# Kernel optimization log

Hardware: AMD Instinct MI355X
Metric: run time of the kernel (lower is better)

The kernel has to match this reference:

```python
import jax, jax.numpy as jnp
import numpy as np


def setup_inputs() -> dict:
    key = jax.random.key(0)
    k1, k2 = jax.random.split(key)
    x = jax.random.normal(k1, (4, 2048, 512), dtype=jnp.float32)
    proxy = jax.random.normal(k2, (16, 512), dtype=jnp.float32)
    return {"x": x, "proxy": proxy}


def reference(x, proxy):
    # x: (B, S, D), proxy: (P, D)
    num_proxies = proxy.shape[0]
    # prods: (B, P, S) = proxy @ x^T per batch
    prods = jnp.einsum('pd,bsd->bps', proxy, x)
    # broadcast outer product: (B, P, S, D), then running prefix sum over seq
    y = jnp.cumsum(prods[..., None] * x[:, None, :, :], axis=2)
    # softmax gate over proxies (dim=1), scaled by sqrt(P)
    w = jax.nn.softmax(prods / jnp.sqrt(jnp.float32(num_proxies)), axis=1)
    # weighted sum over proxies -> (B, S, D)
    out = jnp.einsum('bps,bpsd->bsd', w, y)
    return out
```

## Files before the change

### kernel.cpp

```cpp
#include <hip/hip_runtime.h>
#include <hip/hip_bf16.h>

#define B 4
#define S 2048
#define D 512
#define P 16
#define NC 64
#define CL 32

__global__ __launch_bounds__(256) void k_prods(const float* __restrict__ x,
                                               const float* __restrict__ proxy,
                                               float* __restrict__ prods,
                                               float* __restrict__ wgt) {
    const int wave = (blockIdx.x * blockDim.x + threadIdx.x) >> 6;
    const int lane = threadIdx.x & 63;
    const int bs0  = wave * 4;

    float4 pA[P], pB[P];
#pragma unroll
    for (int p = 0; p < P; ++p) {
        const float* pr = proxy + p * D + lane * 8;
        pA[p] = *(const float4*)pr;
        pB[p] = *(const float4*)(pr + 4);
    }

#pragma unroll
    for (int r = 0; r < 4; ++r) {
        const int bs = bs0 + r;
        const float* xr = x + (size_t)bs * D + lane * 8;
        float4 xa = *(const float4*)xr;
        float4 xb = *(const float4*)(xr + 4);

        float part[P];
#pragma unroll
        for (int p = 0; p < P; ++p) {
            part[p] = xa.x*pA[p].x + xa.y*pA[p].y + xa.z*pA[p].z + xa.w*pA[p].w
                    + xb.x*pB[p].x + xb.y*pB[p].y + xb.z*pB[p].z + xb.w*pB[p].w;
        }

        float a8[8];
#pragma unroll
        for (int k = 0; k < 8; ++k) {
            bool hi = lane & 1;
            float mine = hi ? part[2*k+1] : part[2*k];
            float oth  = hi ? part[2*k]   : part[2*k+1];
            a8[k] = mine + __shfl_xor(oth, 1);
        }
        float a4[4];
#pragma unroll
        for (int k = 0; k < 4; ++k) {
            bool hi = lane & 2;
            float mine = hi ? a8[2*k+1] : a8[2*k];
            float oth  = hi ? a8[2*k]   : a8[2*k+1];
            a4[k] = mine + __shfl_xor(oth, 2);
        }
        float a2[2];
#pragma unroll
        for (int k = 0; k < 2; ++k) {
            bool hi = lane & 4;
            float mine = hi ? a4[2*k+1] : a4[2*k];
            float oth  = hi ? a4[2*k]   : a4[2*k+1];
            a2[k] = mine + __shfl_xor(oth, 4);
        }
        float a1;
        {
            bool hi = lane & 8;
            float mine = hi ? a2[1] : a2[0];
            float oth  = hi ? a2[0] : a2[1];
            a1 = mine + __shfl_xor(oth, 8);
        }
        a1 += __shfl_xor(a1, 16);
        a1 += __shfl_xor(a1, 32);

        float m = a1;
#pragma unroll
        for (int off = 1; off < 16; off <<= 1) m = fmaxf(m, __shfl_xor(m, off));
        float e = __expf((a1 - m) * 0.25f);
        float den = e;
#pragma unroll
        for (int off = 1; off < 16; off <<= 1) den += __shfl_xor(den, off);

        if (lane < P) {
            prods[(size_t)bs * P + lane] = a1;
            wgt  [(size_t)bs * P + lane] = e / den;
        }
    }
}

__global__ __launch_bounds__(256) void k_totals(const float* __restrict__ x,
                                                const float* __restrict__ prods,
                                                float* __restrict__ T) {
    int h = blockIdx.x & 1;
    int c = (blockIdx.x >> 1) & (NC - 1);
    int b = blockIdx.x >> 7;
    int d = h * 256 + threadIdx.x;

    float acc[P];
#pragma unroll
    for (int p = 0; p < P; ++p) acc[p] = 0.f;

    int bs0 = b * S + c * CL;
#pragma unroll 4
    for (int i = 0; i < CL; ++i) {
        int bs = bs0 + i;
        float xv = x[(size_t)bs * D + d];
        const float4* pp = (const float4*)(prods + (size_t)bs * P);
        float pr[P];
        ((float4*)pr)[0] = pp[0];
        ((float4*)pr)[1] = pp[1];
        ((float4*)pr)[2] = pp[2];
        ((float4*)pr)[3] = pp[3];
#pragma unroll
        for (int p = 0; p < P; ++p) acc[p] = fmaf(pr[p], xv, acc[p]);
    }
    size_t tb = ((size_t)(b * NC + c)) * (P * D) + d;
#pragma unroll
    for (int p = 0; p < P; ++p) T[tb + p * D] = acc[p];
}

__global__ __launch_bounds__(256) void k_scan(float* __restrict__ T) {
    int t = blockIdx.x * blockDim.x + threadIdx.x;
    int d = t & (D - 1);
    int p = (t >> 9) & (P - 1);
    int b = t >> 13;
    size_t base = ((size_t)b * NC * P + p) * D + d;
    float run = 0.f;
#pragma unroll 8
    for (int c = 0; c < NC; ++c) {
        size_t idx = base + (size_t)c * (P * D);
        float v = T[idx];
        T[idx] = run;
        run += v;
    }
}

__global__ __launch_bounds__(256) void k_apply(const float* __restrict__ x,
                                               const float* __restrict__ prods,
                                               const float* __restrict__ wgt,
                                               const float* __restrict__ T,
                                               float* __restrict__ out) {
    __shared__ float s_pw[2][CL][P];

    int h = blockIdx.x & 1;
    int c = (blockIdx.x >> 1) & (NC - 1);
    int b = blockIdx.x >> 7;
    int d = h * 256 + threadIdx.x;
    int bs0 = b * S + c * CL;

    {
        int t = threadIdx.x;
        if (t < 128) {
            ((float4*)&s_pw[0][0][0])[t] =
                ((const float4*)(prods + (size_t)bs0 * P))[t];
        } else {
            ((float4*)&s_pw[1][0][0])[t - 128] =
                ((const float4*)(wgt + (size_t)bs0 * P))[t - 128];
        }
    }

    float xv[CL];
#pragma unroll
    for (int i = 0; i < CL; ++i) xv[i] = x[(size_t)(bs0 + i) * D + d];

    float st[P];
    size_t tb = ((size_t)(b * NC + c)) * (P * D) + d;
#pragma unroll
    for (int p = 0; p < P; ++p) st[p] = T[tb + p * D];

    __syncthreads();

#pragma unroll
    for (int i = 0; i < CL; ++i) {
        float pr[P], ww[P];
        const float4* sp = (const float4*)&s_pw[0][i][0];
        const float4* sw = (const float4*)&s_pw[1][i][0];
        ((float4*)pr)[0] = sp[0];
        ((float4*)pr)[1] = sp[1];
        ((float4*)pr)[2] = sp[2];
        ((float4*)pr)[3] = sp[3];
        ((float4*)ww)[0] = sw[0];
        ((float4*)ww)[1] = sw[1];
        ((float4*)ww)[2] = sw[2];
        ((float4*)ww)[3] = sw[3];
        float o = 0.f;
#pragma unroll
        for (int p = 0; p < P; ++p) {
            st[p] = fmaf(pr[p], xv[i], st[p]);
            o = fmaf(ww[p], st[p], o);
        }
        out[(size_t)(bs0 + i) * D + d] = o;
    }
}

extern "C" void kernel_launch(void* const* d_in, const int* in_sizes, int n_in,
                              void* d_out, int out_size, void* d_ws, size_t ws_size,
                              hipStream_t stream) {
    const float* x     = (const float*)d_in[0];
    const float* proxy = (const float*)d_in[1];
    float* out   = (float*)d_out;

    float* prods = (float*)d_ws;
    float* wgt   = prods + (size_t)B * S * P;
    float* T     = wgt   + (size_t)B * S * P;

    k_prods <<<(B * S) / 16,      256, 0, stream>>>(x, proxy, prods, wgt);
    k_totals<<<B * NC * 2,        256, 0, stream>>>(x, prods, T);
    k_scan  <<<(B * P * D) / 256, 256, 0, stream>>>(T);
    k_apply <<<B * NC * 2,        256, 0, stream>>>(x, prods, wgt, T, out);
}
```

Measured before the change: 35.76 us.

## Fuse proxy products and chunk totals into one kernel via shared memory

Merges the projection/softmax kernel and the per-chunk totals kernel into one 512-thread block per chunk. Products are kept in shared memory and reused for the chunk totals, which drops one launch and the global re-read of the products. In exchange there are only 256 blocks of 512 threads, the x chunk is read twice within the block, and the register pressure is high, so occupancy may drop.

```diff
diff --git a/kernel.cpp b/kernel.cpp
--- a/kernel.cpp
+++ b/kernel.cpp
@@ -8,114 +8,123 @@
 #define NC 64
 #define CL 32
 
-__global__ __launch_bounds__(256) void k_prods(const float* __restrict__ x,
-                                               const float* __restrict__ proxy,
-                                               float* __restrict__ prods,
-                                               float* __restrict__ wgt) {
-    const int wave = (blockIdx.x * blockDim.x + threadIdx.x) >> 6;
-    const int lane = threadIdx.x & 63;
-    const int bs0  = wave * 4;
-
-    float4 pA[P], pB[P];
-#pragma unroll
-    for (int p = 0; p < P; ++p) {
-        const float* pr = proxy + p * D + lane * 8;
-        pA[p] = *(const float4*)pr;
-        pB[p] = *(const float4*)(pr + 4);
-    }
-
-#pragma unroll
-    for (int r = 0; r < 4; ++r) {
-        const int bs = bs0 + r;
-        const float* xr = x + (size_t)bs * D + lane * 8;
-        float4 xa = *(const float4*)xr;
-        float4 xb = *(const float4*)(xr + 4);
-
-        float part[P];
+__global__ __launch_bounds__(512) void k_pt(const float* __restrict__ x,
+                                            const float* __restrict__ proxy,
+                                            float* __restrict__ prods,
+                                            float* __restrict__ wgt,
+                                            float* __restrict__ T) {
+    __shared__ float s_pr[CL][P];
+    __shared__ float s_w [CL][P];
+
+    const int c    = blockIdx.x & (NC - 1);
+    const int b    = blockIdx.x >> 6;
+    const int tid  = threadIdx.x;
+    const int lane = tid & 63;
+    const int wv   = tid >> 6;
+    const int bs0  = b * S + c * CL;
+
+    {
+        float4 pA[P], pB[P];
 #pragma unroll
         for (int p = 0; p < P; ++p) {
-            part[p] = xa.x*pA[p].x + xa.y*pA[p].y + xa.z*pA[p].z + xa.w*pA[p].w
-                    + xb.x*pB[p].x + xb.y*pB[p].y + xb.z*pB[p].z + xb.w*pB[p].w;
-        }
-
-        float a8[8];
-#pragma unroll
-        for (int k = 0; k < 8; ++k) {
-            bool hi = lane & 1;
-            float mine = hi ? part[2*k+1] : part[2*k];
-            float oth  = hi ? part[2*k]   : part[2*k+1];
-            a8[k] = mine + __shfl_xor(oth, 1);
-        }
-        float a4[4];
-#pragma unroll
-        for (int k = 0; k < 4; ++k) {
-            bool hi = lane & 2;
-            float mine = hi ? a8[2*k+1] : a8[2*k];
-            float oth  = hi ? a8[2*k]   : a8[2*k+1];
-            a4[k] = mine + __shfl_xor(oth, 2);
-        }
-        float a2[2];
-#pragma unroll
-        for (int k = 0; k < 2; ++k) {
-            bool hi = lane & 4;
-            float mine = hi ? a4[2*k+1] : a4[2*k];
-            float oth  = hi ? a4[2*k]   : a4[2*k+1];
-            a2[k] = mine + __shfl_xor(oth, 4);
-        }
-        float a1;
-        {
-            bool hi = lane & 8;
-            float mine = hi ? a2[1] : a2[0];
-            float oth  = hi ? a2[0] : a2[1];
-            a1 = mine + __shfl_xor(oth, 8);
-        }
-        a1 += __shfl_xor(a1, 16);
-        a1 += __shfl_xor(a1, 32);
-
-        float m = a1;
-#pragma unroll
-        for (int off = 1; off < 16; off <<= 1) m = fmaxf(m, __shfl_xor(m, off));
-        float e = __expf((a1 - m) * 0.25f);
-        float den = e;
-#pragma unroll
-        for (int off = 1; off < 16; off <<= 1) den += __shfl_xor(den, off);
-
-        if (lane < P) {
-            prods[(size_t)bs * P + lane] = a1;
-            wgt  [(size_t)bs * P + lane] = e / den;
-        }
-    }
-}
-
-__global__ __launch_bounds__(256) void k_totals(const float* __restrict__ x,
-                                                const float* __restrict__ prods,
-                                                float* __restrict__ T) {
-    int h = blockIdx.x & 1;
-    int c = (blockIdx.x >> 1) & (NC - 1);
-    int b = blockIdx.x >> 7;
-    int d = h * 256 + threadIdx.x;
-
-    float acc[P];
-#pragma unroll
-    for (int p = 0; p < P; ++p) acc[p] = 0.f;
-
-    int bs0 = b * S + c * CL;
-#pragma unroll 4
-    for (int i = 0; i < CL; ++i) {
-        int bs = bs0 + i;
-        float xv = x[(size_t)bs * D + d];
-        const float4* pp = (const float4*)(prods + (size_t)bs * P);
-        float pr[P];
-        ((float4*)pr)[0] = pp[0];
-        ((float4*)pr)[1] = pp[1];
-        ((float4*)pr)[2] = pp[2];
-        ((float4*)pr)[3] = pp[3];
-#pragma unroll
-        for (int p = 0; p < P; ++p) acc[p] = fmaf(pr[p], xv, acc[p]);
-    }
-    size_t tb = ((size_t)(b * NC + c)) * (P * D) + d;
-#pragma unroll
-    for (int p = 0; p < P; ++p) T[tb + p * D] = acc[p];
+            const float* pr = proxy + p * D + lane * 8;
+            pA[p] = *(const float4*)pr;
+            pB[p] = *(const float4*)(pr + 4);
+        }
+
+#pragma unroll
+        for (int r = 0; r < 4; ++r) {
+            const int sl = wv * 4 + r;
+            const int bs = bs0 + sl;
+            const float* xr = x + (size_t)bs * D + lane * 8;
+            float4 xa = *(const float4*)xr;
+            float4 xb = *(const float4*)(xr + 4);
+
+            float part[P];
+#pragma unroll
+            for (int p = 0; p < P; ++p) {
+                part[p] = xa.x*pA[p].x + xa.y*pA[p].y + xa.z*pA[p].z + xa.w*pA[p].w
+                        + xb.x*pB[p].x + xb.y*pB[p].y + xb.z*pB[p].z + xb.w*pB[p].w;
+            }
+
+            float a8[8];
+#pragma unroll
+            for (int k = 0; k < 8; ++k) {
+                bool hi = lane & 1;
+                float mine = hi ? part[2*k+1] : part[2*k];
+                float oth  = hi ? part[2*k]   : part[2*k+1];
+                a8[k] = mine + __shfl_xor(oth, 1);
+            }
+            float a4[4];
+#pragma unroll
+            for (int k = 0; k < 4; ++k) {
+                bool hi = lane & 2;
+                float mine = hi ? a8[2*k+1] : a8[2*k];
+                float oth  = hi ? a8[2*k]   : a8[2*k+1];
+                a4[k] = mine + __shfl_xor(oth, 2);
+            }
+            float a2[2];
+#pragma unroll
+            for (int k = 0; k < 2; ++k) {
+                bool hi = lane & 4;
+                float mine = hi ? a4[2*k+1] : a4[2*k];
+                float oth  = hi ? a4[2*k]   : a4[2*k+1];
+                a2[k] = mine + __shfl_xor(oth, 4);
+            }
+            float a1;
+            {
+                bool hi = lane & 8;
+                float mine = hi ? a2[1] : a2[0];
+                float oth  = hi ? a2[0] : a2[1];
+                a1 = mine + __shfl_xor(oth, 8);
+            }
+            a1 += __shfl_xor(a1, 16);
+            a1 += __shfl_xor(a1, 32);
+
+            float m = a1;
+#pragma unroll
+            for (int off = 1; off < 16; off <<= 1) m = fmaxf(m, __shfl_xor(m, off));
+            float e = __expf((a1 - m) * 0.25f);
+            float den = e;
+#pragma unroll
+            for (int off = 1; off < 16; off <<= 1) den += __shfl_xor(den, off);
+
+            if (lane < P) {
+                float w = e / den;
+                s_pr[sl][lane] = a1;
+                s_w [sl][lane] = w;
+                prods[(size_t)bs * P + lane] = a1;
+                wgt  [(size_t)bs * P + lane] = w;
+            }
+        }
+    }
+    __syncthreads();
+
+    {
+        const int d = tid;
+        float xv[CL];
+#pragma unroll
+        for (int i = 0; i < CL; ++i) xv[i] = x[(size_t)(bs0 + i) * D + d];
+
+        float acc[P];
+#pragma unroll
+        for (int p = 0; p < P; ++p) acc[p] = 0.f;
+
+#pragma unroll
+        for (int i = 0; i < CL; ++i) {
+            float pr[P];
+            const float4* sp = (const float4*)&s_pr[i][0];
+            ((float4*)pr)[0] = sp[0];
+            ((float4*)pr)[1] = sp[1];
+            ((float4*)pr)[2] = sp[2];
+            ((float4*)pr)[3] = sp[3];
+#pragma unroll
+            for (int p = 0; p < P; ++p) acc[p] = fmaf(pr[p], xv[i], acc[p]);
+        }
+        size_t tb = (size_t)blockIdx.x * (P * D) + d;
+#pragma unroll
+        for (int p = 0; p < P; ++p) T[tb + p * D] = acc[p];
+    }
 }
 
 __global__ __launch_bounds__(256) void k_scan(float* __restrict__ T) {
@@ -203,8 +212,7 @@
     float* wgt   = prods + (size_t)B * S * P;
     float* T     = wgt   + (size_t)B * S * P;
 
-    k_prods <<<(B * S) / 16,      256, 0, stream>>>(x, proxy, prods, wgt);
-    k_totals<<<B * NC * 2,        256, 0, stream>>>(x, prods, T);
-    k_scan  <<<(B * P * D) / 256, 256, 0, stream>>>(T);
-    k_apply <<<B * NC * 2,        256, 0, stream>>>(x, prods, wgt, T, out);
-}
+    k_pt   <<<B * NC,             512, 0, stream>>>(x, proxy, prods, wgt, T);
+    k_scan <<<(B * P * D) / 256,  256, 0, stream>>>(T);
+    k_apply<<<B * NC * 2,         256, 0, stream>>>(x, prods, wgt, T, out);
+}
```

Result: no change. 36.01 us (+0.7%).
